# Kernel tuning notes

Measured on AMD Instinct MI355X. Metric: run time of the kernel, lower is better.

The kernel has to match this reference:

```python
import jax, jax.numpy as jnp
import numpy as np
from functools import partial

N_NODES = 100000
N_EDGES = 1600000
N_LABEL = 200000
D = 128


def _add_self_loops(edge_index, edge_weight, num_nodes):
    # PyG GCNConv default: add self loops with fill_value = 1.0
    loops = jnp.arange(num_nodes, dtype=edge_index.dtype)
    src = jnp.concatenate([edge_index[0], loops])
    dst = jnp.concatenate([edge_index[1], loops])
    ew = jnp.concatenate([edge_weight, jnp.ones((num_nodes,), edge_weight.dtype)])
    return src, dst, ew


def _gcn_norm(src, dst, ew, num_nodes):
    # symmetric normalization: D^-1/2 A D^-1/2, degrees over target index
    deg = jax.ops.segment_sum(ew, dst, num_segments=num_nodes)
    dinv = jnp.where(deg > 0, jax.lax.rsqrt(deg), 0.0)
    return dinv[src] * ew * dinv[dst]


def _gcn_conv(x, W, b, src, dst, norm, num_nodes):
    h = x @ W                      # [N, D] small GEMM
    msg = h[src] * norm[:, None]   # gather + scale, [E+N, D]
    out = jax.ops.segment_sum(msg, dst, num_segments=num_nodes)
    return out + b


def setup_inputs() -> dict:
    key = jax.random.key(0)
    ks = jax.random.split(key, 10)
    s = 1.0 / np.sqrt(D)
    return {
        "x": jax.random.normal(ks[0], (N_NODES, D), jnp.float32),
        "edge_index": jax.random.randint(ks[1], (2, N_EDGES), 0, N_NODES, jnp.int64),
        "edge_weight": jax.random.uniform(ks[2], (N_EDGES,), jnp.float32),
        "edge_label_index": jax.random.randint(ks[3], (2, N_LABEL), 0, N_NODES, jnp.int64),
        "W1": jax.random.uniform(ks[4], (D, D), jnp.float32, -s, s),
        "b1": jnp.zeros((D,), jnp.float32),
        "W2": jax.random.uniform(ks[5], (D, D), jnp.float32, -s, s),
        "b2": jnp.zeros((D,), jnp.float32),
        "lin_W": jax.random.uniform(ks[6], (D, D), jnp.float32, -s, s),
        "lin_b": jax.random.uniform(ks[7], (D,), jnp.float32, -s, s),
    }


def reference(x, edge_index, edge_weight, edge_label_index, W1, b1, W2, b2, lin_W, lin_b):
    n = x.shape[0]
    src, dst, ew = _add_self_loops(edge_index, edge_weight, n)
    norm = _gcn_norm(src, dst, ew, n)
    out = jax.nn.relu(_gcn_conv(x, W1, b1, src, dst, norm, n))
    out = jax.nn.relu(_gcn_conv(out, W2, b2, src, dst, norm, n))
    had = out[edge_label_index[0]] * out[edge_label_index[1]]  # [EL, D]
    # lin then sum over features == had @ lin_W @ 1 + sum(lin_b)
    return jnp.sum(had @ lin_W + lin_b, axis=-1)
```

## Files before the change

kernel.cpp:

```cpp
#include <hip/hip_runtime.h>

#define N_NODES 100000
#define N_EDGES 1600000
#define N_LABEL 200000
#define D 128

#define SCAN_BLOCKS ((N_NODES + 255) / 256)

typedef __attribute__((ext_vector_type(8))) short short8;
typedef __attribute__((ext_vector_type(4))) float f32x4;

static __device__ __forceinline__ unsigned short f2bf(float f) {
    unsigned u = __float_as_uint(f);
    u += 0x7fffu + ((u >> 16) & 1u);
    return (unsigned short)(u >> 16);
}
static __device__ __forceinline__ float bf2f_lo(unsigned p) {
    return __uint_as_float(p << 16);
}
static __device__ __forceinline__ float bf2f_hi(unsigned p) {
    return __uint_as_float(p & 0xffff0000u);
}

__global__ void k_prepall(const float* __restrict__ linW, const float* __restrict__ linb,
                          const float* __restrict__ W1, const float* __restrict__ W2,
                          float* __restrict__ wv, float* __restrict__ cval,
                          unsigned short* __restrict__ w1t,
                          unsigned short* __restrict__ w2t,
                          int* __restrict__ cnt8) {
    int b = blockIdx.x;
    if (b == 0) {
        int t = threadIdx.x;
        if (t < 128) {
            float s = 0.f;
            for (int j = 0; j < D; ++j) s += linW[t * D + j];
            wv[t] = s;
        }
        __shared__ float red[128];
        if (t < 128) red[t] = linb[t];
        __syncthreads();
        for (int st = 64; st > 0; st >>= 1) {
            if (t < st) red[t] += red[t + st];
            __syncthreads();
        }
        if (t == 0) *cval = red[0];
    } else if (b <= 64) {
        int i = (b - 1) * 256 + threadIdx.x;
        int k = i >> 7, n = i & 127;
        w1t[n * D + k] = f2bf(W1[i]);
    } else if (b <= 128) {
        int i = (b - 65) * 256 + threadIdx.x;
        int k = i >> 7, n = i & 127;
        w2t[n * D + k] = f2bf(W2[i]);
    } else {
        int i = (b - 129) * 256 + threadIdx.x;
        if (i < 8 * N_NODES) cnt8[i] = 0;
    }
}

__global__ void k_count(const int* __restrict__ ei, int* __restrict__ cnt8,
                        int* __restrict__ rank) {
    int e = blockIdx.x * 256 + threadIdx.x;
    int p = blockIdx.x & 7;
    if (e < N_EDGES) rank[e] = atomicAdd(&cnt8[p * N_NODES + ei[N_EDGES + e]], 1);
}

__global__ void k_scan1(const int* __restrict__ cnt8, int* __restrict__ offs,
                        int* __restrict__ bsum) {
    __shared__ int sm[256];
    int tid = threadIdx.x;
    int i = blockIdx.x * 256 + tid;
    int v = 0;
    if (i < N_NODES) {
#pragma unroll
        for (int q = 0; q < 8; ++q) v += cnt8[q * N_NODES + i];
    }
    sm[tid] = v;
    __syncthreads();
    for (int st = 1; st < 256; st <<= 1) {
        int add = (tid >= st) ? sm[tid - st] : 0;
        __syncthreads();
        sm[tid] += add;
        __syncthreads();
    }
    if (i < N_NODES) offs[i] = sm[tid] - v;
    if (tid == 255) bsum[blockIdx.x] = sm[255];
}

__global__ void k_scan3(int* __restrict__ offs, const int* __restrict__ bsum,
                        const int* __restrict__ cnt8, int* __restrict__ pofs) {
    __shared__ int preSm;
    int tid = threadIdx.x;
    if (tid < 64) {
        int s = 0;
        for (int j = tid; j < (int)blockIdx.x; j += 64) s += bsum[j];
#pragma unroll
        for (int st = 32; st > 0; st >>= 1) s += __shfl_down(s, st, 64);
        if (tid == 0) preSm = s;
    }
    __syncthreads();
    int pre = preSm;
    int i = blockIdx.x * 256 + tid;
    if (i < N_NODES) {
        int base = offs[i] + pre;
        offs[i] = base;
#pragma unroll
        for (int q = 0; q < 8; ++q) {
            pofs[q * N_NODES + i] = base;
            base += cnt8[q * N_NODES + i];
        }
    }
    if (i == 0) offs[N_NODES] = N_EDGES;
}

__global__ void k_scatter(const int* __restrict__ ei, const float* __restrict__ ew,
                          const int* __restrict__ pofs, const int* __restrict__ rank,
                          int2* __restrict__ csr) {
    int e = blockIdx.x * 256 + threadIdx.x;
    int p = blockIdx.x & 7;
    if (e < N_EDGES) {
        int d = ei[N_EDGES + e];
        int pos = pofs[p * N_NODES + d] + rank[e];
        csr[pos] = make_int2(ei[e] << 6, __float_as_int(ew[e]));
    }
}

__global__ __launch_bounds__(256) void k_gemm1d(const float* __restrict__ X,
                                                const unsigned short* __restrict__ Wt,
                                                const int* __restrict__ offs,
                                                const int2* __restrict__ csr,
                                                float* __restrict__ dinv,
                                                unsigned short* __restrict__ H) {
    __shared__ unsigned short xs[64 * 128];
    __shared__ unsigned short wts[128 * 128];
    __shared__ float dsm[64];
    int tid = threadIdx.x;
    int lane = tid & 63;
    int rowBase = blockIdx.x * 64;
    int w = __builtin_amdgcn_readfirstlane(tid >> 6);

    for (int t = 0; t < 16; ++t) {
        int node = rowBase + w * 16 + t;
        float dv = 0.f;
        if (node < N_NODES) {
            int p0 = offs[node], p1 = offs[node + 1];
            float s = 0.f;
            for (int pp = p0 + lane; pp < p1; pp += 64)
                s += __int_as_float(csr[pp].y);
#pragma unroll
            for (int st = 32; st > 0; st >>= 1) s += __shfl_xor(s, st, 64);
            dv = rsqrtf(1.0f + s);
            if (lane == 0) dinv[node] = dv;
        }
        if (lane == 0) dsm[w * 16 + t] = dv;
    }

#pragma unroll
    for (int i = 0; i < 4; ++i) {
        int idx = tid + i * 256;
        int r = idx >> 4;
        int kc = (idx & 15) << 3;
        int gr = rowBase + r;
        uint4 pk = make_uint4(0, 0, 0, 0);
        if (gr < N_NODES) {
            float4 v0 = *(const float4*)&X[(size_t)gr * D + kc];
            float4 v1 = *(const float4*)&X[(size_t)gr * D + kc + 4];
            pk.x = (unsigned)f2bf(v0.x) | ((unsigned)f2bf(v0.y) << 16);
            pk.y = (unsigned)f2bf(v0.z) | ((unsigned)f2bf(v0.w) << 16);
            pk.z = (unsigned)f2bf(v1.x) | ((unsigned)f2bf(v1.y) << 16);
            pk.w = (unsigned)f2bf(v1.z) | ((unsigned)f2bf(v1.w) << 16);
        }
        *(uint4*)&xs[(r * D + kc) ^ ((r & 7) << 3)] = pk;
    }
#pragma unroll
    for (int i = 0; i < 8; ++i) {
        int idx = tid + i * 256;
        int n = idx >> 4;
        int kc = (idx & 15) << 3;
        uint4 pk = *(const uint4*)&Wt[n * D + kc];
        *(uint4*)&wts[(n * D + kc) ^ ((n & 7) << 3)] = pk;
    }
    __syncthreads();

    int wrow = w * 16;
    int l15 = lane & 15;
    int l4 = (lane >> 4) << 2;

    f32x4 acc[8] = {};
    union FragU { short8 v; uint2 u2[2]; };

#pragma unroll
    for (int kk = 0; kk < 4; ++kk) {
        int kb = kk * 32 + l4;
        int m = wrow + l15;
        FragU a;
        a.u2[0] = *(uint2*)&xs[(m * D + kb) ^ ((m & 7) << 3)];
        a.u2[1] = *(uint2*)&xs[(m * D + kb + 16) ^ ((m & 7) << 3)];
#pragma unroll
        for (int ct = 0; ct < 8; ++ct) {
            int n = ct * 16 + l15;
            FragU b;
            b.u2[0] = *(uint2*)&wts[(n * D + kb) ^ ((n & 7) << 3)];
            b.u2[1] = *(uint2*)&wts[(n * D + kb + 16) ^ ((n & 7) << 3)];
            acc[ct] = __builtin_amdgcn_mfma_f32_16x16x32_bf16(a.v, b.v, acc[ct], 0, 0, 0);
        }
    }

    int rloc = wrow + l4;
    float dn[4];
#pragma unroll
    for (int r = 0; r < 4; ++r) dn[r] = dsm[rloc + r];
#pragma unroll
    for (int ct = 0; ct < 8; ++ct) {
#pragma unroll
        for (int r = 0; r < 4; ++r) {
            int gr = rowBase + rloc + r;
            if (gr < N_NODES)
                H[(size_t)gr * D + ct * 16 + l15] = f2bf(acc[ct][r] * dn[r]);
        }
    }
}

__global__ __launch_bounds__(256) void k_agg_gemm(const unsigned* __restrict__ h,
                                                  const float* __restrict__ dinv,
                                                  const int* __restrict__ offs,
                                                  const int2* __restrict__ csr,
                                                  const float* __restrict__ bias,
                                                  const unsigned short* __restrict__ Wt,
                                                  unsigned short* __restrict__ H) {
    __shared__ unsigned short xs[64 * 128];
    int tid = threadIdx.x;
    int lane = tid & 63;
    int rowBase = blockIdx.x * 64;
    int w = __builtin_amdgcn_readfirstlane(tid >> 6);

    float2 bb = *(const float2*)&bias[lane * 2];
    for (int t = 0; t < 16; ++t) {
        int nodeLoc = w * 16 + t;
        int node = rowBase + nodeLoc;
        unsigned val = 0;
        if (node < N_NODES) {
            int p0 = offs[node], p1 = offs[node + 1];
            float a0 = 0.f, a1 = 0.f;
            for (int p = p0; p < p1; p += 8) {
                int2 cc[8];
                float ww[8];
#pragma unroll
                for (int k = 0; k < 8; ++k) {
                    int pe = p + k;
                    bool v = pe < p1;
                    cc[k] = csr[v ? pe : p0];
                    ww[k] = v ? __int_as_float(cc[k].y) : 0.f;
                }
                unsigned hh[8];
#pragma unroll
                for (int k = 0; k < 8; ++k)
                    hh[k] = h[(size_t)(unsigned)cc[k].x + lane];
#pragma unroll
                for (int k = 0; k < 8; ++k) {
                    a0 += ww[k] * bf2f_lo(hh[k]);
                    a1 += ww[k] * bf2f_hi(hh[k]);
                }
            }
            unsigned sv = h[(size_t)node * 64 + lane];
            a0 += bf2f_lo(sv);
            a1 += bf2f_hi(sv);
            float dnn = dinv[node];
            a0 = fmaxf(a0 * dnn + bb.x, 0.f);
            a1 = fmaxf(a1 * dnn + bb.y, 0.f);
            val = (unsigned)f2bf(a0) | ((unsigned)f2bf(a1) << 16);
        }
        *(unsigned*)&xs[((nodeLoc * D) + (lane << 1)) ^ ((nodeLoc & 7) << 3)] = val;
    }

    int wrow = w * 16;
    int l15 = lane & 15;
    int l4 = (lane >> 4) << 2;

    f32x4 acc[8] = {};
    union FragU { short8 v; uint2 u2[2]; };

#pragma unroll
    for (int kk = 0; kk < 4; ++kk) {
        int kb = kk * 32 + l4;
        int m = wrow + l15;
        FragU a;
        a.u2[0] = *(uint2*)&xs[(m * D + kb) ^ ((m & 7) << 3)];
        a.u2[1] = *(uint2*)&xs[(m * D + kb + 16) ^ ((m & 7) << 3)];
#pragma unroll
        for (int ct = 0; ct < 8; ++ct) {
            int n = ct * 16 + l15;
            FragU b;
            b.u2[0] = *(const uint2*)&Wt[n * D + kb];
            b.u2[1] = *(const uint2*)&Wt[n * D + kb + 16];
            acc[ct] = __builtin_amdgcn_mfma_f32_16x16x32_bf16(a.v, b.v, acc[ct], 0, 0, 0);
        }
    }

    int rloc = wrow + l4;
    float dn[4];
#pragma unroll
    for (int r = 0; r < 4; ++r) {
        int gr = rowBase + rloc + r;
        dn[r] = (gr < N_NODES) ? dinv[gr] : 0.f;
    }
#pragma unroll
    for (int ct = 0; ct < 8; ++ct) {
#pragma unroll
        for (int r = 0; r < 4; ++r) {
            int gr = rowBase + rloc + r;
            if (gr < N_NODES)
                H[(size_t)gr * D + ct * 16 + l15] = f2bf(acc[ct][r] * dn[r]);
        }
    }
}

__global__ __launch_bounds__(256) void k_agg(const unsigned* __restrict__ h,
                                             const float* __restrict__ dinv,
                                             const int* __restrict__ offs,
                                             const int2* __restrict__ csr,
                                             const float* __restrict__ bias,
                                             unsigned* __restrict__ out) {
    int lane = threadIdx.x & 63;
    int node = __builtin_amdgcn_readfirstlane(blockIdx.x * 4 + (threadIdx.x >> 6));
    if (node >= N_NODES) return;

    int p0 = offs[node], p1 = offs[node + 1];
    float a0 = 0.f, a1 = 0.f;

    for (int p = p0; p < p1; p += 8) {
        int2 cc[8];
        float ww[8];
#pragma unroll
        for (int k = 0; k < 8; ++k) {
            int pe = p + k;
            bool v = pe < p1;
            cc[k] = csr[v ? pe : p0];
            ww[k] = v ? __int_as_float(cc[k].y) : 0.f;
        }
        unsigned hh[8];
#pragma unroll
        for (int k = 0; k < 8; ++k)
            hh[k] = h[(size_t)(unsigned)cc[k].x + lane];
#pragma unroll
        for (int k = 0; k < 8; ++k) {
            a0 += ww[k] * bf2f_lo(hh[k]);
            a1 += ww[k] * bf2f_hi(hh[k]);
        }
    }

    unsigned sv = h[(size_t)node * 64 + lane];
    a0 += bf2f_lo(sv);
    a1 += bf2f_hi(sv);
    float dn = dinv[node];
    float2 bb = *(const float2*)&bias[lane * 2];
    a0 = fmaxf(a0 * dn + bb.x, 0.f);
    a1 = fmaxf(a1 * dn + bb.y, 0.f);
    out[(size_t)node * 64 + lane] = (unsigned)f2bf(a0) | ((unsigned)f2bf(a1) << 16);
}

__global__ void k_final(const int* __restrict__ eli, const unsigned* __restrict__ o2,
                        const float* __restrict__ wv, const float* __restrict__ cval,
                        float* __restrict__ res) {
    unsigned g = blockIdx.x * 256 + threadIdx.x;
    int l = g >> 5;
    int t = g & 31;
    if (l < N_LABEL) {
        int a = eli[l];
        int b = eli[N_LABEL + l];
        uint2 ua = *(const uint2*)&o2[(size_t)a * 64 + t * 2];
        uint2 ub = *(const uint2*)&o2[(size_t)b * 64 + t * 2];
        float4 w4 = *(const float4*)&wv[t * 4];
        float s = bf2f_lo(ua.x) * bf2f_lo(ub.x) * w4.x
                + bf2f_hi(ua.x) * bf2f_hi(ub.x) * w4.y
                + bf2f_lo(ua.y) * bf2f_lo(ub.y) * w4.z
                + bf2f_hi(ua.y) * bf2f_hi(ub.y) * w4.w;
#pragma unroll
        for (int st = 16; st > 0; st >>= 1) s += __shfl_down(s, st, 32);
        if (t == 0) res[l] = s + *cval;
    }
}

extern "C" void kernel_launch(void* const* d_in, const int* in_sizes, int n_in,
                              void* d_out, int out_size, void* d_ws, size_t ws_size,
                              hipStream_t stream) {
    const float* x    = (const float*)d_in[0];
    const int*   ei   = (const int*)d_in[1];
    const float* ew   = (const float*)d_in[2];
    const int*   eli  = (const int*)d_in[3];
    const float* W1   = (const float*)d_in[4];
    const float* b1   = (const float*)d_in[5];
    const float* W2   = (const float*)d_in[6];
    const float* b2   = (const float*)d_in[7];
    const float* linW = (const float*)d_in[8];
    const float* linb = (const float*)d_in[9];
    float* res = (float*)d_out;

    float*          ws    = (float*)d_ws;
    float*          dinv  = ws;
    int*            offs  = (int*)(dinv + N_NODES);
    int*            bsum  = offs + N_NODES + 4;
    int*            cnt8  = bsum + 512;
    int*            pofs  = cnt8 + 8 * N_NODES;
    int2*           csr   = (int2*)(pofs + 8 * N_NODES);
    unsigned*       h_bf  = (unsigned*)(csr + N_EDGES);
    unsigned*       h2    = h_bf + (size_t)N_NODES * 64;
    unsigned*       out2  = h2 + (size_t)N_NODES * 64;
    float*          wv    = (float*)(out2 + (size_t)N_NODES * 64);
    float*          cval  = wv + D;
    unsigned short* w1t   = (unsigned short*)(cval + 1);
    unsigned short* w2t   = w1t + D * D;
    int*            rank  = (int*)h2;

    k_prepall<<<129 + (8 * N_NODES + 255) / 256, 256, 0, stream>>>(
        linW, linb, W1, W2, wv, cval, w1t, w2t, cnt8);

    k_count<<<(N_EDGES + 255) / 256, 256, 0, stream>>>(ei, cnt8, rank);
    k_scan1<<<SCAN_BLOCKS, 256, 0, stream>>>(cnt8, offs, bsum);
    k_scan3<<<SCAN_BLOCKS, 256, 0, stream>>>(offs, bsum, cnt8, pofs);
    k_scatter<<<(N_EDGES + 255) / 256, 256, 0, stream>>>(ei, ew, pofs, rank, csr);

    const int GB = (N_NODES + 63) / 64;

    k_gemm1d<<<GB, 256, 0, stream>>>(x, w1t, offs, csr, dinv, (unsigned short*)h_bf);

    k_agg_gemm<<<GB, 256, 0, stream>>>(h_bf, dinv, offs, csr, b1, w2t,
                                       (unsigned short*)h2);

    k_agg<<<(N_NODES + 3) / 4, 256, 0, stream>>>(h2, dinv, offs, csr, b2, out2);

    k_final<<<(N_LABEL * 32 + 255) / 256, 256, 0, stream>>>(eli, out2, wv, cval, res);
}
```

Measured before the change: 402.2 us.

## Split fused aggregate+GEMM into separate agg kernel and LDS-staged GEMM

Replaces the fused layer-2 aggregation+GEMM kernel with the existing per-node aggregation kernel (4 nodes per block) followed by a standalone GEMM that stages both the input tile and the transposed weight in LDS with swizzling. The fused kernel had each wave walk 16 nodes serially, which gives poor latency hiding for the irregular gathers. Splitting it adds a full write and re-read of the intermediate bf16 feature matrix through global memory plus one extra launch, in exchange for better parallelism in the gather phase.

```diff
diff --git a/kernel.cpp b/kernel.cpp
--- a/kernel.cpp
+++ b/kernel.cpp
@@ -221,59 +221,38 @@
     }
 }
 
-__global__ __launch_bounds__(256) void k_agg_gemm(const unsigned* __restrict__ h,
-                                                  const float* __restrict__ dinv,
-                                                  const int* __restrict__ offs,
-                                                  const int2* __restrict__ csr,
-                                                  const float* __restrict__ bias,
-                                                  const unsigned short* __restrict__ Wt,
-                                                  unsigned short* __restrict__ H) {
+__global__ __launch_bounds__(256) void k_gemm(const unsigned short* __restrict__ IN,
+                                              const unsigned short* __restrict__ Wt,
+                                              const float* __restrict__ dinv,
+                                              unsigned short* __restrict__ H) {
     __shared__ unsigned short xs[64 * 128];
+    __shared__ unsigned short wts[128 * 128];
     int tid = threadIdx.x;
+    int rowBase = blockIdx.x * 64;
+
+#pragma unroll
+    for (int i = 0; i < 4; ++i) {
+        int idx = tid + i * 256;
+        int r = idx >> 4;
+        int kc = (idx & 15) << 3;
+        int gr = rowBase + r;
+        uint4 pk = make_uint4(0, 0, 0, 0);
+        if (gr < N_NODES)
+            pk = *(const uint4*)&IN[(size_t)gr * D + kc];
+        *(uint4*)&xs[(r * D + kc) ^ ((r & 7) << 3)] = pk;
+    }
+#pragma unroll
+    for (int i = 0; i < 8; ++i) {
+        int idx = tid + i * 256;
+        int n = idx >> 4;
+        int kc = (idx & 15) << 3;
+        uint4 pk = *(const uint4*)&Wt[n * D + kc];
+        *(uint4*)&wts[(n * D + kc) ^ ((n & 7) << 3)] = pk;
+    }
+    __syncthreads();
+
     int lane = tid & 63;
-    int rowBase = blockIdx.x * 64;
-    int w = __builtin_amdgcn_readfirstlane(tid >> 6);
-
-    float2 bb = *(const float2*)&bias[lane * 2];
-    for (int t = 0; t < 16; ++t) {
-        int nodeLoc = w * 16 + t;
-        int node = rowBase + nodeLoc;
-        unsigned val = 0;
-        if (node < N_NODES) {
-            int p0 = offs[node], p1 = offs[node + 1];
-            float a0 = 0.f, a1 = 0.f;
-            for (int p = p0; p < p1; p += 8) {
-                int2 cc[8];
-                float ww[8];
-#pragma unroll
-                for (int k = 0; k < 8; ++k) {
-                    int pe = p + k;
-                    bool v = pe < p1;
-                    cc[k] = csr[v ? pe : p0];
-                    ww[k] = v ? __int_as_float(cc[k].y) : 0.f;
-                }
-                unsigned hh[8];
-#pragma unroll
-                for (int k = 0; k < 8; ++k)
-                    hh[k] = h[(size_t)(unsigned)cc[k].x + lane];
-#pragma unroll
-                for (int k = 0; k < 8; ++k) {
-                    a0 += ww[k] * bf2f_lo(hh[k]);
-                    a1 += ww[k] * bf2f_hi(hh[k]);
-                }
-            }
-            unsigned sv = h[(size_t)node * 64 + lane];
-            a0 += bf2f_lo(sv);
-            a1 += bf2f_hi(sv);
-            float dnn = dinv[node];
-            a0 = fmaxf(a0 * dnn + bb.x, 0.f);
-            a1 = fmaxf(a1 * dnn + bb.y, 0.f);
-            val = (unsigned)f2bf(a0) | ((unsigned)f2bf(a1) << 16);
-        }
-        *(unsigned*)&xs[((nodeLoc * D) + (lane << 1)) ^ ((nodeLoc & 7) << 3)] = val;
-    }
-
-    int wrow = w * 16;
+    int wrow = (tid >> 6) * 16;
     int l15 = lane & 15;
     int l4 = (lane >> 4) << 2;
 
@@ -291,8 +270,8 @@
         for (int ct = 0; ct < 8; ++ct) {
             int n = ct * 16 + l15;
             FragU b;
-            b.u2[0] = *(const uint2*)&Wt[n * D + kb];
-            b.u2[1] = *(const uint2*)&Wt[n * D + kb + 16];
+            b.u2[0] = *(uint2*)&wts[(n * D + kb) ^ ((n & 7) << 3)];
+            b.u2[1] = *(uint2*)&wts[(n * D + kb + 16) ^ ((n & 7) << 3)];
             acc[ct] = __builtin_amdgcn_mfma_f32_16x16x32_bf16(a.v, b.v, acc[ct], 0, 0, 0);
         }
     }
@@ -404,13 +383,13 @@
     int*            pofs  = cnt8 + 8 * N_NODES;
     int2*           csr   = (int2*)(pofs + 8 * N_NODES);
     unsigned*       h_bf  = (unsigned*)(csr + N_EDGES);
-    unsigned*       h2    = h_bf + (size_t)N_NODES * 64;
-    unsigned*       out2  = h2 + (size_t)N_NODES * 64;
+    unsigned*       agg   = h_bf + (size_t)N_NODES * 64;
+    unsigned*       out2  = agg + (size_t)N_NODES * 64;
     float*          wv    = (float*)(out2 + (size_t)N_NODES * 64);
     float*          cval  = wv + D;
     unsigned short* w1t   = (unsigned short*)(cval + 1);
     unsigned short* w2t   = w1t + D * D;
-    int*            rank  = (int*)h2;
+    int*            rank  = (int*)agg;
 
     k_prepall<<<129 + (8 * N_NODES + 255) / 256, 256, 0, stream>>>(
         linW, linb, W1, W2, wv, cval, w1t, w2t, cnt8);
@@ -423,11 +402,11 @@
     const int GB = (N_NODES + 63) / 64;
 
     k_gemm1d<<<GB, 256, 0, stream>>>(x, w1t, offs, csr, dinv, (unsigned short*)h_bf);
-
-    k_agg_gemm<<<GB, 256, 0, stream>>>(h_bf, dinv, offs, csr, b1, w2t,
-                                       (unsigned short*)h2);
-
-    k_agg<<<(N_NODES + 3) / 4, 256, 0, stream>>>(h2, dinv, offs, csr, b2, out2);
+    k_agg<<<(N_NODES + 3) / 4, 256, 0, stream>>>(h_bf, dinv, offs, csr, b1, agg);
+
+    k_gemm<<<GB, 256, 0, stream>>>((unsigned short*)agg, w2t, dinv,
+                                   (unsigned short*)h_bf);
+    k_agg<<<(N_NODES + 3) / 4, 256, 0, stream>>>(h_bf, dinv, offs, csr, b2, out2);
 
     k_final<<<(N_LABEL * 32 + 255) / 256, 256, 0, stream>>>(eli, out2, wv, cval, res);
 }
```

Result: faster. 362.9 us (-9.8%).
